# Kernel optimization log

Measured on AMD Instinct MI355X. Metric: run time of the kernel, lower is better.

The kernel has to match this reference:

```python
import jax, jax.numpy as jnp
import numpy as np

N = 50000      # nodes
E = 800000     # edges (avg degree 16)
D_IN = 128     # input_dim
H = 64         # hidden_dim (== output_dim)
L = 3          # num_layers


def setup_inputs() -> dict:
    key = jax.random.key(0)
    ks = jax.random.split(key, 24)
    s = 0.05
    p = lambda k, shape: jax.random.normal(k, shape, dtype=jnp.float32) * s
    inp = {}
    inp["node_features"] = jax.random.normal(ks[0], (N, D_IN), dtype=jnp.float32)
    inp["edge_index"] = jax.random.randint(ks[1], (2, E), 0, N, dtype=jnp.int32)
    # pre_mlp: Linear-ReLU-Linear (setup_LRL_nn with hidden_sizes=[hidden_dim])
    inp["pre_w1"] = p(ks[2], (D_IN, H)); inp["pre_b1"] = jnp.zeros((H,), jnp.float32)
    inp["pre_w2"] = p(ks[3], (H, H));    inp["pre_b2"] = jnp.zeros((H,), jnp.float32)
    # learnable skip gates (initialized to ones as in the module)
    inp["skip"] = jnp.ones((L, L), jnp.float32)
    # SAGEConv layers: lin_l (on mean-aggregated neighbors, with bias) + lin_r (root)
    for i in range(L):
        din = H * (i + 1)
        inp[f"wl{i}"] = p(ks[4 + 3 * i], (din, H))
        inp[f"bl{i}"] = jnp.zeros((H,), jnp.float32)
        inp[f"wr{i}"] = p(ks[5 + 3 * i], (din, H))
    # post_mlp: 256->64, 64->64, 64->256, 256->64
    inp["post_w1"] = p(ks[14], (H * (L + 1), H)); inp["post_b1"] = jnp.zeros((H,), jnp.float32)
    inp["post_w2"] = p(ks[15], (H, H));           inp["post_b2"] = jnp.zeros((H,), jnp.float32)
    inp["post_w3"] = p(ks[16], (H, 256));         inp["post_b3"] = jnp.zeros((256,), jnp.float32)
    inp["post_w4"] = p(ks[17], (256, H));         inp["post_b4"] = jnp.zeros((H,), jnp.float32)
    return inp


def _sage(x, src, dst, inv_deg, wl, bl, wr):
    # PyG SAGEConv (mean aggr): lin_l(mean_{j->i} x_j) + lin_r(x_i)
    agg = jax.ops.segment_sum(x[src], dst, num_segments=N) * inv_deg  # [N, Din]
    return agg @ wl + bl + x @ wr


def reference(node_features, edge_index,
              pre_w1, pre_b1, pre_w2, pre_b2, skip,
              wl0, bl0, wr0, wl1, bl1, wr1, wl2, bl2, wr2,
              post_w1, post_b1, post_w2, post_b2, post_w3, post_b3, post_w4, post_b4):
    src, dst = edge_index[0], edge_index[1]
    deg = jax.ops.segment_sum(jnp.ones((E,), jnp.float32), dst, num_segments=N)
    inv_deg = (1.0 / jnp.maximum(deg, 1.0))[:, None]  # [N,1]

    # pre_mlp
    x = jax.nn.relu(node_features @ pre_w1 + pre_b1) @ pre_w2 + pre_b2  # [N,H]

    layers = [(wl0, bl0, wr0), (wl1, bl1, wr1), (wl2, bl2, wr2)]
    all_emb = [x]
    emb = x
    for i, (wl, bl, wr) in enumerate(layers):
        gates = jax.nn.sigmoid(skip[i, :i + 1])  # [i+1]
        curr = jnp.concatenate([all_emb[j] * gates[j] for j in range(i + 1)], axis=1)  # [N, H*(i+1)]
        h = jax.nn.relu(_sage(curr, src, dst, inv_deg, wl, bl, wr))  # [N,H]  (dropout p=0)
        emb = jnp.concatenate([emb, h], axis=1)
        all_emb.append(h)

    s = jnp.sum(emb, axis=-2)  # sums over all nodes -> [H*(L+1)] (faithful to source)
    h = jax.nn.leaky_relu(s @ post_w1 + post_b1, negative_slope=0.1)
    h = jax.nn.relu(h @ post_w2 + post_b2)
    h = jax.nn.relu(h @ post_w3 + post_b3)
    return h @ post_w4 + post_b4  # [H]
```

## Files before the change

### kernel.cpp

```cpp
#include <hip/hip_runtime.h>
#include <math.h>

#define NN 50000
#define NE 800000
#define NB 196

typedef float v4f __attribute__((ext_vector_type(4)));
typedef float v2f __attribute__((ext_vector_type(2)));
typedef _Float16 v8h __attribute__((ext_vector_type(8)));

__device__ __forceinline__ unsigned char enc8(float v) {
#if __has_builtin(__builtin_amdgcn_cvt_pk_fp8_f32)
  return (unsigned char)(__builtin_amdgcn_cvt_pk_fp8_f32(v, v, 0, false) & 0xFF);
#else
  unsigned u = __float_as_uint(v);
  unsigned s = (u >> 24) & 0x80u;
  unsigned au = u & 0x7fffffffu;
  float a = __uint_as_float(au);
  if (au < 0x3C800000u) {
    int m = (int)(a * 512.0f + 0.5f);
    if (m >= 8) return (unsigned char)(s | 8u);
    return (unsigned char)(s | (unsigned)m);
  }
  unsigned r = au + 0x7FFFFu + ((au >> 20) & 1u);
  unsigned e = (r >> 23) - 120u;
  unsigned man = (r >> 20) & 7u;
  if (e > 15u) { e = 15u; man = 6u; }
  return (unsigned char)(s | (e << 3) | man);
#endif
}

#if __has_builtin(__builtin_amdgcn_cvt_pk_f32_fp8)
#define DEC8_HW 1
#else
__device__ __forceinline__ float dec8_1(unsigned b) {
  unsigned s = (b & 0x80u) << 24;
  unsigned em = b & 0x7fu;
  float v;
  if (em >= 8u) v = __uint_as_float((((em >> 3) + 120u) << 23) | ((em & 7u) << 20));
  else v = (float)em * 0.001953125f;
  return __uint_as_float(__float_as_uint(v) | s);
}
#endif

__device__ __forceinline__ void dec8x8(uint2 u, float* f) {
#ifdef DEC8_HW
  v2f p0 = __builtin_amdgcn_cvt_pk_f32_fp8((int)u.x, false);
  v2f p1 = __builtin_amdgcn_cvt_pk_f32_fp8((int)u.x, true);
  v2f p2 = __builtin_amdgcn_cvt_pk_f32_fp8((int)u.y, false);
  v2f p3 = __builtin_amdgcn_cvt_pk_f32_fp8((int)u.y, true);
  f[0] = p0.x; f[1] = p0.y; f[2] = p1.x; f[3] = p1.y;
  f[4] = p2.x; f[5] = p2.y; f[6] = p3.x; f[7] = p3.y;
#else
#pragma unroll
  for (int i = 0; i < 4; ++i) f[i] = dec8_1((u.x >> (8 * i)) & 0xFF);
#pragma unroll
  for (int i = 0; i < 4; ++i) f[4 + i] = dec8_1((u.y >> (8 * i)) & 0xFF);
#endif
}
__device__ __forceinline__ void dec8x16(uint4 u, float* f) {
  dec8x8(make_uint2(u.x, u.y), f);
  dec8x8(make_uint2(u.z, u.w), f + 8);
}


__global__ __launch_bounds__(256) void k_bhist(const int* __restrict__ dst,
                                               int* __restrict__ gbcnt) {
  __shared__ int lcnt[NB];
  int t = threadIdx.x;
  for (int i = t; i < NB; i += 256) lcnt[i] = 0;
  __syncthreads();
  int eb = blockIdx.x * 4096;
#pragma unroll
  for (int i = 0; i < 16; ++i) {
    int e = eb + i * 256 + t;
    if (e < NE) atomicAdd(&lcnt[dst[e] >> 8], 1);
  }
  __syncthreads();
  for (int i = t; i < NB; i += 256)
    if (lcnt[i]) atomicAdd(&gbcnt[i], lcnt[i]);
}

__global__ __launch_bounds__(256) void k_bscan(const int* __restrict__ gbcnt,
                                               int* __restrict__ boff,
                                               int* __restrict__ gcur,
                                               int* __restrict__ offs,
                                               float* __restrict__ sv) {
  __shared__ int sd[256];
  int t = threadIdx.x;
  sv[t] = 0.f;
  int v = (t < NB) ? gbcnt[t] : 0;
  sd[t] = v;
  __syncthreads();
  for (int o = 1; o < 256; o <<= 1) {
    int u = (t >= o) ? sd[t - o] : 0;
    __syncthreads();
    sd[t] += u;
    __syncthreads();
  }
  if (t < NB) { int x = sd[t] - v; boff[t] = x; gcur[t] = x; }
  if (t == NB - 1) boff[NB] = sd[t];
  if (t == 0) offs[NN] = NE;
}

__global__ __launch_bounds__(256) void k_bscatter(const int* __restrict__ src,
                                                  const int* __restrict__ dst,
                                                  int* __restrict__ gcur,
                                                  unsigned* __restrict__ ebuf) {
  __shared__ int cnt[NB];
  __shared__ int base[NB];
  int t = threadIdx.x;
  for (int i = t; i < NB; i += 256) cnt[i] = 0;
  __syncthreads();
  int eb = blockIdx.x * 4096;
  unsigned pk[16];
  int bk[16], lp[16];
#pragma unroll
  for (int i = 0; i < 16; ++i) {
    int e = eb + i * 256 + t;
    if (e < NE) {
      int d = dst[e];
      int b = d >> 8;
      pk[i] = ((unsigned)src[e] << 8) | (unsigned)(d & 255);
      bk[i] = b;
      lp[i] = atomicAdd(&cnt[b], 1);
    }
  }
  __syncthreads();
  for (int i = t; i < NB; i += 256)
    base[i] = cnt[i] ? atomicAdd(&gcur[i], cnt[i]) : 0;
  __syncthreads();
#pragma unroll
  for (int i = 0; i < 16; ++i) {
    int e = eb + i * 256 + t;
    if (e < NE) ebuf[base[bk[i]] + lp[i]] = pk[i];
  }
}

__global__ __launch_bounds__(256) void k_bbuild(const unsigned* __restrict__ ebuf,
                                                const int* __restrict__ boff,
                                                int* __restrict__ offs,
                                                float* __restrict__ invd,
                                                int* __restrict__ csr) {
  __shared__ int dcnt[256];
  __shared__ int cur[256];
  int t = threadIdx.x;
  int b = blockIdx.x;
  int node0 = b << 8;
  int es = boff[b], ee = boff[b + 1];
  dcnt[t] = 0;
  __syncthreads();
  for (int e = es + t; e < ee; e += 256) atomicAdd(&dcnt[ebuf[e] & 255], 1);
  __syncthreads();
  int v = dcnt[t];
  cur[t] = v;
  __syncthreads();
  for (int o = 1; o < 256; o <<= 1) {
    int u = (t >= o) ? cur[t - o] : 0;
    __syncthreads();
    cur[t] += u;
    __syncthreads();
  }
  int excl = cur[t] - v;
  int node = node0 + t;
  if (node < NN) {
    offs[node] = es + excl;
    invd[node] = 1.0f / fmaxf((float)v, 1.0f);
  }
  __syncthreads();
  cur[t] = es + excl;
  __syncthreads();
  for (int e = es + t; e < ee; e += 256) {
    unsigned pk = ebuf[e];
    int p = atomicAdd(&cur[pk & 255], 1);
    csr[p] = (int)(pk >> 8);
  }
}

struct LinArgs {
  const _Float16* a[6];
  const float* w[6];
  int gidx[6];
  int nsrc;
  int fusedsrc;
  const unsigned char* feat8;
  const int* offs;
  const int* csr;
  const float* invd;
  _Float16* mout;
  const float* bias;
  const float* skip;
  _Float16* outp;
  unsigned char* out8;
  float* colsum;
  int n;
  int relu;
};

__global__ __launch_bounds__(256) void k_linear(LinArgs A) {
  __shared__ _Float16 sW[2][2][64 * 72];
  __shared__ _Float16 atile[64 * 72];
  const int t    = threadIdx.x;
  const int lane = t & 63;
  const int wv   = t >> 6;
  const int qd   = lane >> 4;
  const int ln   = lane & 15;
  const int n0   = blockIdx.x * 64;

  const int sn = t & 63;
  float wreg[16];
  auto loadW = [&](int s) {
    const float* w = A.w[s];
#pragma unroll
    for (int c = 0; c < 2; ++c) {
      int kb = (wv + 4 * c) * 8;
#pragma unroll
      for (int j = 0; j < 8; ++j)
        wreg[c * 8 + j] = w[(size_t)(kb + j) * 64 + sn];
    }
  };
  auto writeW = [&](int s, int b) {
    float gs = 1.0f;
    if (A.gidx[s] >= 0) gs = 1.0f / (1.0f + __expf(-A.skip[A.gidx[s]]));
#pragma unroll
    for (int c = 0; c < 2; ++c) {
      int cb = wv + 4 * c;
      v8h hv, lv;
#pragma unroll
      for (int j = 0; j < 8; ++j) {
        float f = wreg[c * 8 + j] * gs;
        _Float16 h = (_Float16)f;
        hv[j] = h;
        lv[j] = (_Float16)(f - (float)h);
      }
      *(v8h*)(&sW[b][0][sn * 72 + cb * 8]) = hv;
      *(v8h*)(&sW[b][1][sn * 72 + cb * 8]) = lv;
    }
  };

  loadW(0);

  if (A.fusedsrc >= 0) {
    const int nd = t >> 2;
    const int q  = t & 3;
    const int node = n0 + nd;
    float a[16];
#pragma unroll
    for (int i = 0; i < 16; ++i) a[i] = 0.f;
    float dinv = 0.f;
    if (node < A.n) {
      int s = A.offs[node], e = A.offs[node + 1];
      dinv = A.invd[node];
      const unsigned char* fb = A.feat8;
      int p = s;
      for (; p + 4 <= e; p += 4) {
        int j0 = __builtin_nontemporal_load(A.csr + p);
        int j1 = __builtin_nontemporal_load(A.csr + p + 1);
        int j2 = __builtin_nontemporal_load(A.csr + p + 2);
        int j3 = __builtin_nontemporal_load(A.csr + p + 3);
        uint4 u0 = *(const uint4*)(fb + (size_t)j0 * 64 + q * 16);
        uint4 u1 = *(const uint4*)(fb + (size_t)j1 * 64 + q * 16);
        uint4 u2 = *(const uint4*)(fb + (size_t)j2 * 64 + q * 16);
        uint4 u3 = *(const uint4*)(fb + (size_t)j3 * 64 + q * 16);
        float f0[16], f1[16], f2[16], f3[16];
        dec8x16(u0, f0); dec8x16(u1, f1); dec8x16(u2, f2); dec8x16(u3, f3);
#pragma unroll
        for (int i = 0; i < 16; ++i) a[i] += (f0[i] + f1[i]) + (f2[i] + f3[i]);
      }
      for (; p < e; ++p) {
        int j = __builtin_nontemporal_load(A.csr + p);
        uint4 u = *(const uint4*)(fb + (size_t)j * 64 + q * 16);
        float f[16];
        dec8x16(u, f);
#pragma unroll
        for (int i = 0; i < 16; ++i) a[i] += f[i];
      }
    }
    v8h o0, o1;
#pragma unroll
    for (int i = 0; i < 8; ++i) {
      o0[i] = (_Float16)(a[i] * dinv);
      o1[i] = (_Float16)(a[8 + i] * dinv);
    }
    *(v8h*)(&atile[nd * 72 + q * 16]) = o0;
    *(v8h*)(&atile[nd * 72 + q * 16 + 8]) = o1;
    if (A.mout && node < A.n) {
      *(v8h*)(A.mout + (size_t)node * 64 + q * 16) = o0;
      *(v8h*)(A.mout + (size_t)node * 64 + q * 16 + 8) = o1;
    }
  }

  writeW(0, 0);
  __syncthreads();

  v4f acc[4];
#pragma unroll
  for (int ct = 0; ct < 4; ++ct) acc[ct] = (v4f){0.f, 0.f, 0.f, 0.f};

  const int arow = n0 + wv * 16 + ln;
  const bool arv = arow < A.n;
  v8h ah[2];
  auto loadA = [&](int s) {
    if (s == A.fusedsrc) {
      const _Float16* ph = atile + (wv * 16 + ln) * 72;
      ah[0] = *(const v8h*)(ph + qd * 8);
      ah[1] = *(const v8h*)(ph + 32 + qd * 8);
    } else if (arv) {
      const _Float16* ph = A.a[s] + (size_t)arow * 64;
#pragma unroll
      for (int ks = 0; ks < 2; ++ks)
        ah[ks] = *(const v8h*)(ph + ks * 32 + qd * 8);
    } else {
      v8h z;
#pragma unroll
      for (int j = 0; j < 8; ++j) z[j] = (_Float16)0.f;
      ah[0] = ah[1] = z;
    }
  };

  for (int s = 0; s < A.nsrc; ++s) {
    loadA(s);
    if (s + 1 < A.nsrc) loadW(s + 1);
    const _Float16* wh = &sW[s & 1][0][0];
    const _Float16* wl = &sW[s & 1][1][0];
#pragma unroll
    for (int ks = 0; ks < 2; ++ks) {
#pragma unroll
      for (int ct = 0; ct < 4; ++ct) {
        int wn = ct * 16 + ln;
        v8h bh = *(const v8h*)(wh + wn * 72 + ks * 32 + qd * 8);
        v8h bl = *(const v8h*)(wl + wn * 72 + ks * 32 + qd * 8);
        acc[ct] = __builtin_amdgcn_mfma_f32_16x16x32_f16(ah[ks], bh, acc[ct], 0, 0, 0);
        acc[ct] = __builtin_amdgcn_mfma_f32_16x16x32_f16(ah[ks], bl, acc[ct], 0, 0, 0);
      }
    }
    if (s + 1 < A.nsrc) writeW(s + 1, (s + 1) & 1);
    __syncthreads();
  }

  float bvals[4];
#pragma unroll
  for (int ct = 0; ct < 4; ++ct) bvals[ct] = A.bias[ct * 16 + ln];

  unsigned char* f8t = (unsigned char*)&sW[1][0][0];
  float* red = (float*)&sW[0][0][0];

  float cs[4] = {0.f, 0.f, 0.f, 0.f};
#pragma unroll
  for (int ct = 0; ct < 4; ++ct) {
#pragma unroll
    for (int r = 0; r < 4; ++r) {
      int nb = wv * 16 + qd * 4 + r;
      int node = n0 + nb;
      float v = acc[ct][r] + bvals[ct];
      if (A.relu) v = fmaxf(v, 0.f);
      if (node < A.n) {
        if (A.outp) A.outp[(size_t)node * 64 + ct * 16 + ln] = (_Float16)v;
        if (A.out8) f8t[nb * 64 + ct * 16 + ln] = enc8(v);
        cs[ct] += v;
      }
    }
  }
  if (A.colsum) {
#pragma unroll
    for (int ct = 0; ct < 4; ++ct) {
      float v = cs[ct];
      v += __shfl_xor(v, 16, 64);
      v += __shfl_xor(v, 32, 64);
      if (qd == 0) red[wv * 64 + ct * 16 + ln] = v;
    }
  }
  if (A.out8 || A.colsum) __syncthreads();
  if (A.out8) {
    int row = t >> 2, ch = t & 3;
    if (n0 + row < A.n) {
      uint4 val = *(const uint4*)(f8t + row * 64 + ch * 16);
      *(uint4*)(A.out8 + (size_t)(n0 + row) * 64 + ch * 16) = val;
    }
  }
  if (A.colsum && t < 64) {
    float ssum = red[t] + red[64 + t] + red[128 + t] + red[192 + t];
    atomicAdd(&A.colsum[t], ssum);
  }
}

__global__ __launch_bounds__(256) void k_pre(
    const float* __restrict__ nf,
    const float* __restrict__ w1, const float* __restrict__ b1,
    const float* __restrict__ w2, const float* __restrict__ b2,
    _Float16* __restrict__ xout, unsigned char* __restrict__ x8,
    float* __restrict__ colsum, int n) {
  __shared__ _Float16 sW[2][2][64 * 72];
  __shared__ _Float16 atile[64 * 72];
  const int t    = threadIdx.x;
  const int lane = t & 63;
  const int wv   = t >> 6;
  const int qd   = lane >> 4;
  const int ln   = lane & 15;
  const int n0   = blockIdx.x * 64;
  const int sn   = t & 63;

  float wreg[16];
  auto loadW = [&](const float* w) {
#pragma unroll
    for (int c = 0; c < 2; ++c) {
      int kb = (wv + 4 * c) * 8;
#pragma unroll
      for (int j = 0; j < 8; ++j)
        wreg[c * 8 + j] = w[(size_t)(kb + j) * 64 + sn];
    }
  };
  auto writeW = [&](int b) {
#pragma unroll
    for (int c = 0; c < 2; ++c) {
      int cb = wv + 4 * c;
      v8h hv, lv;
#pragma unroll
      for (int j = 0; j < 8; ++j) {
        float f = wreg[c * 8 + j];
        _Float16 h = (_Float16)f;
        hv[j] = h;
        lv[j] = (_Float16)(f - (float)h);
      }
      *(v8h*)(&sW[b][0][sn * 72 + cb * 8]) = hv;
      *(v8h*)(&sW[b][1][sn * 72 + cb * 8]) = lv;
    }
  };

  const int arow = n0 + wv * 16 + ln;
  const bool arv = arow < n;
  v4f acc[4];
#pragma unroll
  for (int ct = 0; ct < 4; ++ct) acc[ct] = (v4f){0.f, 0.f, 0.f, 0.f};
  v8h ah[2];

  auto loadAf32 = [&](const float* base) {
#pragma unroll
    for (int ks = 0; ks < 2; ++ks) {
      v8h hv;
      if (arv) {
        const float* p = base + (size_t)arow * 128 + ks * 32 + qd * 8;
        float4 u0 = *(const float4*)(p);
        float4 u1 = *(const float4*)(p + 4);
        hv[0] = (_Float16)u0.x; hv[1] = (_Float16)u0.y;
        hv[2] = (_Float16)u0.z; hv[3] = (_Float16)u0.w;
        hv[4] = (_Float16)u1.x; hv[5] = (_Float16)u1.y;
        hv[6] = (_Float16)u1.z; hv[7] = (_Float16)u1.w;
      } else {
#pragma unroll
        for (int j = 0; j < 8; ++j) hv[j] = (_Float16)0.f;
      }
      ah[ks] = hv;
    }
  };
  auto domfma = [&](int b) {
    const _Float16* wh = &sW[b][0][0];
    const _Float16* wl = &sW[b][1][0];
#pragma unroll
    for (int ks = 0; ks < 2; ++ks) {
#pragma unroll
      for (int ct = 0; ct < 4; ++ct) {
        int wn = ct * 16 + ln;
        v8h bh = *(const v8h*)(wh + wn * 72 + ks * 32 + qd * 8);
        v8h bl = *(const v8h*)(wl + wn * 72 + ks * 32 + qd * 8);
        acc[ct] = __builtin_amdgcn_mfma_f32_16x16x32_f16(ah[ks], bh, acc[ct], 0, 0, 0);
        acc[ct] = __builtin_amdgcn_mfma_f32_16x16x32_f16(ah[ks], bl, acc[ct], 0, 0, 0);
      }
    }
  };

  loadW(w1);
  writeW(0);
  __syncthreads();
  loadAf32(nf);
  loadW(w1 + 64 * 64);
  domfma(0);
  writeW(1);
  __syncthreads();
  loadAf32(nf + 64);
  loadW(w2);
  domfma(1);
  writeW(0);

  float b1v[4];
#pragma unroll
  for (int ct = 0; ct < 4; ++ct) b1v[ct] = b1[ct * 16 + ln];
#pragma unroll
  for (int ct = 0; ct < 4; ++ct) {
#pragma unroll
    for (int r = 0; r < 4; ++r) {
      int nb = wv * 16 + qd * 4 + r;
      float v = fmaxf(acc[ct][r] + b1v[ct], 0.f);
      atile[nb * 72 + ct * 16 + ln] = (_Float16)v;
    }
  }
#pragma unroll
  for (int ct = 0; ct < 4; ++ct) acc[ct] = (v4f){0.f, 0.f, 0.f, 0.f};
  __syncthreads();

  const int trow = wv * 16 + ln;
#pragma unroll
  for (int ks = 0; ks < 2; ++ks)
    ah[ks] = *(const v8h*)(atile + trow * 72 + ks * 32 + qd * 8);
  domfma(0);

  float b2v[4];
#pragma unroll
  for (int ct = 0; ct < 4; ++ct) b2v[ct] = b2[ct * 16 + ln];

  unsigned char* f8t = (unsigned char*)&sW[1][0][0];
  float* red = (float*)&sW[0][0][0];
  float cs[4] = {0.f, 0.f, 0.f, 0.f};
  __syncthreads();
#pragma unroll
  for (int ct = 0; ct < 4; ++ct) {
#pragma unroll
    for (int r = 0; r < 4; ++r) {
      int nb = wv * 16 + qd * 4 + r;
      int node = n0 + nb;
      float v = acc[ct][r] + b2v[ct];
      if (node < n) {
        xout[(size_t)node * 64 + ct * 16 + ln] = (_Float16)v;
        f8t[nb * 64 + ct * 16 + ln] = enc8(v);
        cs[ct] += v;
      }
    }
  }
#pragma unroll
  for (int ct = 0; ct < 4; ++ct) {
    float v = cs[ct];
    v += __shfl_xor(v, 16, 64);
    v += __shfl_xor(v, 32, 64);
    if (qd == 0) red[wv * 64 + ct * 16 + ln] = v;
  }
  __syncthreads();
  {
    int row = t >> 2, ch = t & 3;
    if (n0 + row < n) {
      uint4 val = *(const uint4*)(f8t + row * 64 + ch * 16);
      *(uint4*)(x8 + (size_t)(n0 + row) * 64 + ch * 16) = val;
    }
  }
  if (t < 64) {
    float ssum = red[t] + red[64 + t] + red[128 + t] + red[192 + t];
    atomicAdd(&colsum[t], ssum);
  }
}

__global__ __launch_bounds__(256) void k_post(const float* __restrict__ s,
                                              const float* __restrict__ w1, const float* __restrict__ b1,
                                              const float* __restrict__ w2, const float* __restrict__ b2,
                                              const float* __restrict__ w3, const float* __restrict__ b3,
                                              const float* __restrict__ w4, const float* __restrict__ b4,
                                              float* __restrict__ outp) {
  __shared__ float sh[256], h1[64], h2[64], h3[256];
  int t = threadIdx.x;
  sh[t] = s[t];
  __syncthreads();
  if (t < 64) {
    float a = b1[t];
    for (int k = 0; k < 256; ++k) a += sh[k] * w1[k * 64 + t];
    h1[t] = (a >= 0.f) ? a : 0.1f * a;
  }
  __syncthreads();
  if (t < 64) {
    float a = b2[t];
    for (int k = 0; k < 64; ++k) a += h1[k] * w2[k * 64 + t];
    h2[t] = fmaxf(a, 0.f);
  }
  __syncthreads();
  {
    float a = b3[t];
    for (int k = 0; k < 64; ++k) a += h2[k] * w3[k * 256 + t];
    h3[t] = fmaxf(a, 0.f);
  }
  __syncthreads();
  if (t < 64) {
    float a = b4[t];
    for (int k = 0; k < 256; ++k) a += h3[k] * w4[k * 64 + t];
    outp[t] = a;
  }
}

extern "C" void kernel_launch(void* const* d_in, const int* in_sizes, int n_in,
                              void* d_out, int out_size, void* d_ws, size_t ws_size,
                              hipStream_t stream) {
  const float* nf     = (const float*)d_in[0];
  const int*   ei     = (const int*)d_in[1];
  const float* pre_w1 = (const float*)d_in[2];
  const float* pre_b1 = (const float*)d_in[3];
  const float* pre_w2 = (const float*)d_in[4];
  const float* pre_b2 = (const float*)d_in[5];
  const float* skip   = (const float*)d_in[6];
  const float* wl0 = (const float*)d_in[7],  *bl0 = (const float*)d_in[8],  *wr0 = (const float*)d_in[9];
  const float* wl1 = (const float*)d_in[10], *bl1 = (const float*)d_in[11], *wr1 = (const float*)d_in[12];
  const float* wl2 = (const float*)d_in[13], *bl2 = (const float*)d_in[14], *wr2 = (const float*)d_in[15];
  const float* pw1 = (const float*)d_in[16], *pb1 = (const float*)d_in[17];
  const float* pw2 = (const float*)d_in[18], *pb2 = (const float*)d_in[19];
  const float* pw3 = (const float*)d_in[20], *pb3 = (const float*)d_in[21];
  const float* pw4 = (const float*)d_in[22], *pb4 = (const float*)d_in[23];
  float* out = (float*)d_out;

  const int N = NN, E = NE;

  char* ws = (char*)d_ws;
  size_t pos = 0;
  auto alloc = [&](size_t bytes) {
    char* p = ws + pos;
    pos += (bytes + 255) & ~(size_t)255;
    return (void*)p;
  };
  int*      gbcnt = (int*)alloc((size_t)NB * 4);
  int*      boff  = (int*)alloc((size_t)(NB + 1) * 4);
  int*      gcur  = (int*)alloc((size_t)NB * 4);
  unsigned* ebuf  = (unsigned*)alloc((size_t)E * 4);
  int*      offs  = (int*)alloc((size_t)(N + 1) * 4);
  float*    invd  = (float*)alloc((size_t)N * 4);
  int*      csr   = (int*)alloc((size_t)E * 4);
  const size_t PB = (size_t)N * 64 * 2;
  _Float16* x  = (_Float16*)alloc(PB);
  _Float16* h0 = (_Float16*)alloc(PB);
  _Float16* h1 = (_Float16*)alloc(PB);
  _Float16* m0 = (_Float16*)alloc(PB);
  _Float16* m1 = (_Float16*)alloc(PB);
  unsigned char* f8 = (unsigned char*)alloc((size_t)N * 64);
  float* sv = (float*)alloc(256 * 4);

  hipMemsetAsync(gbcnt, 0, (size_t)NB * 4, stream);

  const int* e_src = ei;
  const int* e_dst = ei + E;
  const int EGRID = (E + 4095) / 4096;
  k_bhist<<<EGRID, 256, 0, stream>>>(e_dst, gbcnt);
  k_bscan<<<1, 256, 0, stream>>>(gbcnt, boff, gcur, offs, sv);
  k_bscatter<<<EGRID, 256, 0, stream>>>(e_src, e_dst, gcur, ebuf);
  k_bbuild<<<NB, 256, 0, stream>>>(ebuf, boff, offs, invd, csr);

  const int LGRID = (N + 63) / 64;
  auto lin = [&](int nsrc, int fusedsrc, _Float16* mout,
                 const _Float16* a0, const float* w0, int g0,
                 const _Float16* a1, const float* w1_, int g1,
                 const _Float16* a2, const float* w2_, int g2,
                 const _Float16* a3, const float* w3_, int g3,
                 const _Float16* a4, const float* w4_, int g4,
                 const _Float16* a5, const float* w5_, int g5,
                 const float* bias, _Float16* op, unsigned char* o8,
                 float* colsum, int relu) {
    LinArgs A;
    A.a[0] = a0; A.a[1] = a1; A.a[2] = a2; A.a[3] = a3; A.a[4] = a4; A.a[5] = a5;
    A.w[0] = w0; A.w[1] = w1_; A.w[2] = w2_; A.w[3] = w3_; A.w[4] = w4_; A.w[5] = w5_;
    A.gidx[0] = g0; A.gidx[1] = g1; A.gidx[2] = g2; A.gidx[3] = g3; A.gidx[4] = g4; A.gidx[5] = g5;
    A.nsrc = nsrc; A.fusedsrc = fusedsrc;
    A.feat8 = f8; A.offs = offs; A.csr = csr; A.invd = invd;
    A.mout = mout;
    A.bias = bias; A.skip = skip;
    A.outp = op; A.out8 = o8; A.colsum = colsum;
    A.n = N; A.relu = relu;
    k_linear<<<LGRID, 256, 0, stream>>>(A);
  };

  k_pre<<<LGRID, 256, 0, stream>>>(nf, pre_w1, pre_b1, pre_w2, pre_b2,
                                   x, f8, sv, N);

  lin(2, 0, m0,
      nullptr, wl0, 0, x, wr0, 0,
      nullptr, nullptr, -1, nullptr, nullptr, -1,
      nullptr, nullptr, -1, nullptr, nullptr, -1,
      bl0, h0, f8, sv + 64, 1);

  lin(4, 1, m1,
      m0, wl1, 3, nullptr, wl1 + 64 * 64, 4,
      x, wr1, 3, h0, wr1 + 64 * 64, 4,
      nullptr, nullptr, -1, nullptr, nullptr, -1,
      bl1, h1, f8, sv + 128, 1);

  lin(6, 2, nullptr,
      m0, wl2, 6, m1, wl2 + 64 * 64, 7, nullptr, wl2 + 128 * 64, 8,
      x, wr2, 6, h0, wr2 + 64 * 64, 7, h1, wr2 + 128 * 64, 8,
      bl2, nullptr, nullptr, sv + 192, 1);

  k_post<<<1, 256, 0, stream>>>(sv, pw1, pb1, pw2, pb2, pw3, pb3, pw4, pb4, out);
}
```

Before: 333.2 us.

## Prepack gated split-fp16 weights once and double threads in linear kernel

```diff
diff --git a/kernel.cpp b/kernel.cpp
--- a/kernel.cpp
+++ b/kernel.cpp
@@ -4,6 +4,7 @@
 #define NN 50000
 #define NE 800000
 #define NB 196
+#define PBH 8192
 
 typedef float v4f __attribute__((ext_vector_type(4)));
 typedef float v2f __attribute__((ext_vector_type(2)));
@@ -177,10 +178,43 @@
   }
 }
 
+struct WPackArgs {
+  const float* w[15];
+  int gidx[15];
+  const float* skip;
+  _Float16* outp;
+};
+
+__global__ __launch_bounds__(256) void k_wpack(WPackArgs A) {
+  __shared__ float sw[4096];
+  int b = blockIdx.x, t = threadIdx.x;
+  const float* w = A.w[b];
+#pragma unroll
+  for (int i = 0; i < 4; ++i)
+    *(float4*)&sw[i * 1024 + t * 4] = *(const float4*)(w + i * 1024 + t * 4);
+  float gs = 1.f;
+  if (A.gidx[b] >= 0) gs = 1.f / (1.f + __expf(-A.skip[A.gidx[b]]));
+  __syncthreads();
+#pragma unroll
+  for (int i = 0; i < 4; ++i) {
+    int u = t * 4 + i;
+    int lane = u & 63, ct = (u >> 6) & 3, hl = (u >> 8) & 1, ks = (u >> 9) & 1;
+    v8h val;
+#pragma unroll
+    for (int j = 0; j < 8; ++j) {
+      int k = ks * 32 + ((lane >> 4) & 3) * 8 + j;
+      int n = ct * 16 + (lane & 15);
+      float f = sw[k * 64 + n] * gs;
+      _Float16 h = (_Float16)f;
+      val[j] = hl ? (_Float16)(f - (float)h) : h;
+    }
+    *(v8h*)(A.outp + (size_t)b * PBH + (size_t)u * 8) = val;
+  }
+}
+
 struct LinArgs {
   const _Float16* a[6];
-  const float* w[6];
-  int gidx[6];
+  int pb[6];
   int nsrc;
   int fusedsrc;
   const unsigned char* feat8;
@@ -188,8 +222,8 @@
   const int* csr;
   const float* invd;
   _Float16* mout;
+  const _Float16* wp;
   const float* bias;
-  const float* skip;
   _Float16* outp;
   unsigned char* out8;
   float* colsum;
@@ -197,8 +231,189 @@
   int relu;
 };
 
-__global__ __launch_bounds__(256) void k_linear(LinArgs A) {
-  __shared__ _Float16 sW[2][2][64 * 72];
+__global__ __launch_bounds__(512) void k_linear(LinArgs A) {
+  __shared__ _Float16 atile[64 * 72];
+  __shared__ float cbuf[64 * 65];
+  const int t    = threadIdx.x;
+  const int lane = t & 63;
+  const int w    = t >> 6;
+  const int wq   = w & 3;
+  const int sg   = w >> 2;
+  const int qd   = lane >> 4;
+  const int ln   = lane & 15;
+  const int n0   = blockIdx.x * 64;
+
+  if (A.fusedsrc >= 0) {
+    const int nd = t >> 3;
+    const int sl = (t >> 2) & 1;
+    const int q  = t & 3;
+    const int node = n0 + nd;
+    float a[16];
+#pragma unroll
+    for (int i = 0; i < 16; ++i) a[i] = 0.f;
+    float dinv = 0.f;
+    if (node < A.n) {
+      int s = A.offs[node], e = A.offs[node + 1];
+      dinv = A.invd[node];
+      const unsigned char* fb = A.feat8;
+      if (e > s) {
+        int emax = e - 1;
+        for (int p0 = s; p0 < e; p0 += 8) {
+          int pa = p0 + sl, pb_ = p0 + 2 + sl, pc = p0 + 4 + sl, pd = p0 + 6 + sl;
+          int ja = __builtin_nontemporal_load(A.csr + (pa < emax ? pa : emax));
+          int jb = __builtin_nontemporal_load(A.csr + (pb_ < emax ? pb_ : emax));
+          int jc = __builtin_nontemporal_load(A.csr + (pc < emax ? pc : emax));
+          int jd = __builtin_nontemporal_load(A.csr + (pd < emax ? pd : emax));
+          uint4 ua = *(const uint4*)(fb + (size_t)ja * 64 + q * 16);
+          uint4 ub = *(const uint4*)(fb + (size_t)jb * 64 + q * 16);
+          uint4 uc = *(const uint4*)(fb + (size_t)jc * 64 + q * 16);
+          uint4 ud = *(const uint4*)(fb + (size_t)jd * 64 + q * 16);
+          float f[16];
+          dec8x16(ua, f);
+          if (pa < e) {
+#pragma unroll
+            for (int i = 0; i < 16; ++i) a[i] += f[i];
+          }
+          dec8x16(ub, f);
+          if (pb_ < e) {
+#pragma unroll
+            for (int i = 0; i < 16; ++i) a[i] += f[i];
+          }
+          dec8x16(uc, f);
+          if (pc < e) {
+#pragma unroll
+            for (int i = 0; i < 16; ++i) a[i] += f[i];
+          }
+          dec8x16(ud, f);
+          if (pd < e) {
+#pragma unroll
+            for (int i = 0; i < 16; ++i) a[i] += f[i];
+          }
+        }
+      }
+    }
+#pragma unroll
+    for (int i = 0; i < 16; ++i) a[i] += __shfl_xor(a[i], 4, 64);
+    if (sl == 0) {
+      v8h o0, o1;
+#pragma unroll
+      for (int i = 0; i < 8; ++i) {
+        o0[i] = (_Float16)(a[i] * dinv);
+        o1[i] = (_Float16)(a[8 + i] * dinv);
+      }
+      *(v8h*)(&atile[nd * 72 + q * 16]) = o0;
+      *(v8h*)(&atile[nd * 72 + q * 16 + 8]) = o1;
+      if (A.mout && node < A.n) {
+        *(v8h*)(A.mout + (size_t)node * 64 + q * 16) = o0;
+        *(v8h*)(A.mout + (size_t)node * 64 + q * 16 + 8) = o1;
+      }
+    }
+  }
+  __syncthreads();
+
+  v4f acc[4];
+#pragma unroll
+  for (int ct = 0; ct < 4; ++ct) acc[ct] = (v4f){0.f, 0.f, 0.f, 0.f};
+
+  const int arow = n0 + wq * 16 + ln;
+  const bool arv = arow < A.n;
+  const int h = (A.nsrc + 1) >> 1;
+  const int sbeg = sg ? h : 0;
+  const int send = sg ? A.nsrc : h;
+  v8h ah[2];
+
+  for (int s = sbeg; s < send; ++s) {
+    if (s == A.fusedsrc) {
+      const _Float16* ph = atile + (wq * 16 + ln) * 72;
+      ah[0] = *(const v8h*)(ph + qd * 8);
+      ah[1] = *(const v8h*)(ph + 32 + qd * 8);
+    } else if (arv) {
+      const _Float16* ph = A.a[s] + (size_t)arow * 64;
+      ah[0] = *(const v8h*)(ph + qd * 8);
+      ah[1] = *(const v8h*)(ph + 32 + qd * 8);
+    } else {
+      v8h z;
+#pragma unroll
+      for (int j = 0; j < 8; ++j) z[j] = (_Float16)0.f;
+      ah[0] = ah[1] = z;
+    }
+    const _Float16* pw = A.wp + (size_t)A.pb[s] * PBH;
+#pragma unroll
+    for (int ks = 0; ks < 2; ++ks) {
+#pragma unroll
+      for (int ct = 0; ct < 4; ++ct) {
+        const _Float16* pf = pw + (size_t)(ks * 512 + ct * 64 + lane) * 8;
+        v8h bh = *(const v8h*)(pf);
+        v8h bl = *(const v8h*)(pf + 256 * 8);
+        acc[ct] = __builtin_amdgcn_mfma_f32_16x16x32_f16(ah[ks], bh, acc[ct], 0, 0, 0);
+        acc[ct] = __builtin_amdgcn_mfma_f32_16x16x32_f16(ah[ks], bl, acc[ct], 0, 0, 0);
+      }
+    }
+  }
+
+  if (sg == 1) {
+#pragma unroll
+    for (int ct = 0; ct < 4; ++ct)
+#pragma unroll
+      for (int r = 0; r < 4; ++r) {
+        int nb = wq * 16 + qd * 4 + r;
+        cbuf[nb * 65 + ct * 16 + ln] = acc[ct][r];
+      }
+  }
+  __syncthreads();
+
+  unsigned char* f8t = (unsigned char*)atile;
+  float* red = (float*)&atile[2304];
+
+  if (sg == 0) {
+    float bvals[4];
+#pragma unroll
+    for (int ct = 0; ct < 4; ++ct) bvals[ct] = A.bias[ct * 16 + ln];
+    float cs[4] = {0.f, 0.f, 0.f, 0.f};
+#pragma unroll
+    for (int ct = 0; ct < 4; ++ct) {
+#pragma unroll
+      for (int r = 0; r < 4; ++r) {
+        int nb = wq * 16 + qd * 4 + r;
+        int node = n0 + nb;
+        float v = acc[ct][r] + cbuf[nb * 65 + ct * 16 + ln] + bvals[ct];
+        if (A.relu) v = fmaxf(v, 0.f);
+        if (node < A.n) {
+          if (A.outp) A.outp[(size_t)node * 64 + ct * 16 + ln] = (_Float16)v;
+          if (A.out8) f8t[nb * 64 + ct * 16 + ln] = enc8(v);
+          cs[ct] += v;
+        }
+      }
+    }
+    if (A.colsum) {
+#pragma unroll
+      for (int ct = 0; ct < 4; ++ct) {
+        float v = cs[ct];
+        v += __shfl_xor(v, 16, 64);
+        v += __shfl_xor(v, 32, 64);
+        if (qd == 0) red[wq * 64 + ct * 16 + ln] = v;
+      }
+    }
+  }
+  if (A.out8 || A.colsum) __syncthreads();
+  if (A.out8 && t < 256) {
+    int row = t >> 2, ch = t & 3;
+    if (n0 + row < A.n) {
+      uint4 val = *(const uint4*)(f8t + row * 64 + ch * 16);
+      *(uint4*)(A.out8 + (size_t)(n0 + row) * 64 + ch * 16) = val;
+    }
+  }
+  if (A.colsum && t < 64) {
+    float ssum = red[t] + red[64 + t] + red[128 + t] + red[192 + t];
+    atomicAdd(&A.colsum[t], ssum);
+  }
+}
+
+__global__ __launch_bounds__(256) void k_pre(
+    const float* __restrict__ nf, const _Float16* __restrict__ wp,
+    const float* __restrict__ b1, const float* __restrict__ b2,
+    _Float16* __restrict__ xout, unsigned char* __restrict__ x8,
+    float* __restrict__ colsum, int n) {
   __shared__ _Float16 atile[64 * 72];
   const int t    = threadIdx.x;
   const int lane = t & 63;
@@ -206,240 +421,35 @@
   const int qd   = lane >> 4;
   const int ln   = lane & 15;
   const int n0   = blockIdx.x * 64;
-
-  const int sn = t & 63;
-  float wreg[16];
-  auto loadW = [&](int s) {
-    const float* w = A.w[s];
-#pragma unroll
-    for (int c = 0; c < 2; ++c) {
-      int kb = (wv + 4 * c) * 8;
-#pragma unroll
-      for (int j = 0; j < 8; ++j)
-        wreg[c * 8 + j] = w[(size_t)(kb + j) * 64 + sn];
-    }
-  };
-  auto writeW = [&](int s, int b) {
-    float gs = 1.0f;
-    if (A.gidx[s] >= 0) gs = 1.0f / (1.0f + __expf(-A.skip[A.gidx[s]]));
-#pragma unroll
-    for (int c = 0; c < 2; ++c) {
-      int cb = wv + 4 * c;
-      v8h hv, lv;
-#pragma unroll
-      for (int j = 0; j < 8; ++j) {
-        float f = wreg[c * 8 + j] * gs;
-        _Float16 h = (_Float16)f;
-        hv[j] = h;
-        lv[j] = (_Float16)(f - (float)h);
-      }
-      *(v8h*)(&sW[b][0][sn * 72 + cb * 8]) = hv;
-      *(v8h*)(&sW[b][1][sn * 72 + cb * 8]) = lv;
-    }
-  };
-
-  loadW(0);
-
-  if (A.fusedsrc >= 0) {
-    const int nd = t >> 2;
-    const int q  = t & 3;
-    const int node = n0 + nd;
-    float a[16];
-#pragma unroll
-    for (int i = 0; i < 16; ++i) a[i] = 0.f;
-    float dinv = 0.f;
-    if (node < A.n) {
-      int s = A.offs[node], e = A.offs[node + 1];
-      dinv = A.invd[node];
-      const unsigned char* fb = A.feat8;
-      int p = s;
-      for (; p + 4 <= e; p += 4) {
-        int j0 = __builtin_nontemporal_load(A.csr + p);
-        int j1 = __builtin_nontemporal_load(A.csr + p + 1);
-        int j2 = __builtin_nontemporal_load(A.csr + p + 2);
-        int j3 = __builtin_nontemporal_load(A.csr + p + 3);
-        uint4 u0 = *(const uint4*)(fb + (size_t)j0 * 64 + q * 16);
-        uint4 u1 = *(const uint4*)(fb + (size_t)j1 * 64 + q * 16);
-        uint4 u2 = *(const uint4*)(fb + (size_t)j2 * 64 + q * 16);
-        uint4 u3 = *(const uint4*)(fb + (size_t)j3 * 64 + q * 16);
-        float f0[16], f1[16], f2[16], f3[16];
-        dec8x16(u0, f0); dec8x16(u1, f1); dec8x16(u2, f2); dec8x16(u3, f3);
-#pragma unroll
-        for (int i = 0; i < 16; ++i) a[i] += (f0[i] + f1[i]) + (f2[i] + f3[i]);
-      }
-      for (; p < e; ++p) {
-        int j = __builtin_nontemporal_load(A.csr + p);
-        uint4 u = *(const uint4*)(fb + (size_t)j * 64 + q * 16);
-        float f[16];
-        dec8x16(u, f);
-#pragma unroll
-        for (int i = 0; i < 16; ++i) a[i] += f[i];
-      }
-    }
-    v8h o0, o1;
-#pragma unroll
-    for (int i = 0; i < 8; ++i) {
-      o0[i] = (_Float16)(a[i] * dinv);
-      o1[i] = (_Float16)(a[8 + i] * dinv);
-    }
-    *(v8h*)(&atile[nd * 72 + q * 16]) = o0;
-    *(v8h*)(&atile[nd * 72 + q * 16 + 8]) = o1;
-    if (A.mout && node < A.n) {
-      *(v8h*)(A.mout + (size_t)node * 64 + q * 16) = o0;
-      *(v8h*)(A.mout + (size_t)node * 64 + q * 16 + 8) = o1;
-    }
-  }
-
-  writeW(0, 0);
-  __syncthreads();
+  const int arow = n0 + wv * 16 + ln;
+  const bool arv = arow < n;
 
   v4f acc[4];
 #pragma unroll
   for (int ct = 0; ct < 4; ++ct) acc[ct] = (v4f){0.f, 0.f, 0.f, 0.f};
-
-  const int arow = n0 + wv * 16 + ln;
-  const bool arv = arow < A.n;
   v8h ah[2];
-  auto loadA = [&](int s) {
-    if (s == A.fusedsrc) {
-      const _Float16* ph = atile + (wv * 16 + ln) * 72;
-      ah[0] = *(const v8h*)(ph + qd * 8);
-      ah[1] = *(const v8h*)(ph + 32 + qd * 8);
-    } else if (arv) {
-      const _Float16* ph = A.a[s] + (size_t)arow * 64;
-#pragma unroll
-      for (int ks = 0; ks < 2; ++ks)
-        ah[ks] = *(const v8h*)(ph + ks * 32 + qd * 8);
-    } else {
-      v8h z;
-#pragma unroll
-      for (int j = 0; j < 8; ++j) z[j] = (_Float16)0.f;
-      ah[0] = ah[1] = z;
-    }
-  };
-
-  for (int s = 0; s < A.nsrc; ++s) {
-    loadA(s);
-    if (s + 1 < A.nsrc) loadW(s + 1);
-    const _Float16* wh = &sW[s & 1][0][0];
-    const _Float16* wl = &sW[s & 1][1][0];
+
+  auto domfma = [&](int pbi) {
+    const _Float16* pw = wp + (size_t)pbi * PBH;
 #pragma unroll
     for (int ks = 0; ks < 2; ++ks) {
 #pragma unroll
       for (int ct = 0; ct < 4; ++ct) {
-        int wn = ct * 16 + ln;
-        v8h bh = *(const v8h*)(wh + wn * 72 + ks * 32 + qd * 8);
-        v8h bl = *(const v8h*)(wl + wn * 72 + ks * 32 + qd * 8);
+        const _Float16* pf = pw + (size_t)(ks * 512 + ct * 64 + lane) * 8;
+        v8h bh = *(const v8h*)(pf);
+        v8h bl = *(const v8h*)(pf + 256 * 8);
         acc[ct] = __builtin_amdgcn_mfma_f32_16x16x32_f16(ah[ks], bh, acc[ct], 0, 0, 0);
         acc[ct] = __builtin_amdgcn_mfma_f32_16x16x32_f16(ah[ks], bl, acc[ct], 0, 0, 0);
       }
     }
-    if (s + 1 < A.nsrc) writeW(s + 1, (s + 1) & 1);
-    __syncthreads();
-  }
-
-  float bvals[4];
-#pragma unroll
-  for (int ct = 0; ct < 4; ++ct) bvals[ct] = A.bias[ct * 16 + ln];
-
-  unsigned char* f8t = (unsigned char*)&sW[1][0][0];
-  float* red = (float*)&sW[0][0][0];
-
-  float cs[4] = {0.f, 0.f, 0.f, 0.f};
-#pragma unroll
-  for (int ct = 0; ct < 4; ++ct) {
-#pragma unroll
-    for (int r = 0; r < 4; ++r) {
-      int nb = wv * 16 + qd * 4 + r;
-      int node = n0 + nb;
-      float v = acc[ct][r] + bvals[ct];
-      if (A.relu) v = fmaxf(v, 0.f);
-      if (node < A.n) {
-        if (A.outp) A.outp[(size_t)node * 64 + ct * 16 + ln] = (_Float16)v;
-        if (A.out8) f8t[nb * 64 + ct * 16 + ln] = enc8(v);
-        cs[ct] += v;
-      }
-    }
-  }
-  if (A.colsum) {
-#pragma unroll
-    for (int ct = 0; ct < 4; ++ct) {
-      float v = cs[ct];
-      v += __shfl_xor(v, 16, 64);
-      v += __shfl_xor(v, 32, 64);
-      if (qd == 0) red[wv * 64 + ct * 16 + ln] = v;
-    }
-  }
-  if (A.out8 || A.colsum) __syncthreads();
-  if (A.out8) {
-    int row = t >> 2, ch = t & 3;
-    if (n0 + row < A.n) {
-      uint4 val = *(const uint4*)(f8t + row * 64 + ch * 16);
-      *(uint4*)(A.out8 + (size_t)(n0 + row) * 64 + ch * 16) = val;
-    }
-  }
-  if (A.colsum && t < 64) {
-    float ssum = red[t] + red[64 + t] + red[128 + t] + red[192 + t];
-    atomicAdd(&A.colsum[t], ssum);
-  }
-}
-
-__global__ __launch_bounds__(256) void k_pre(
-    const float* __restrict__ nf,
-    const float* __restrict__ w1, const float* __restrict__ b1,
-    const float* __restrict__ w2, const float* __restrict__ b2,
-    _Float16* __restrict__ xout, unsigned char* __restrict__ x8,
-    float* __restrict__ colsum, int n) {
-  __shared__ _Float16 sW[2][2][64 * 72];
-  __shared__ _Float16 atile[64 * 72];
-  const int t    = threadIdx.x;
-  const int lane = t & 63;
-  const int wv   = t >> 6;
-  const int qd   = lane >> 4;
-  const int ln   = lane & 15;
-  const int n0   = blockIdx.x * 64;
-  const int sn   = t & 63;
-
-  float wreg[16];
-  auto loadW = [&](const float* w) {
-#pragma unroll
-    for (int c = 0; c < 2; ++c) {
-      int kb = (wv + 4 * c) * 8;
-#pragma unroll
-      for (int j = 0; j < 8; ++j)
-        wreg[c * 8 + j] = w[(size_t)(kb + j) * 64 + sn];
-    }
   };
-  auto writeW = [&](int b) {
-#pragma unroll
-    for (int c = 0; c < 2; ++c) {
-      int cb = wv + 4 * c;
-      v8h hv, lv;
-#pragma unroll
-      for (int j = 0; j < 8; ++j) {
-        float f = wreg[c * 8 + j];
-        _Float16 h = (_Float16)f;
-        hv[j] = h;
-        lv[j] = (_Float16)(f - (float)h);
-      }
-      *(v8h*)(&sW[b][0][sn * 72 + cb * 8]) = hv;
-      *(v8h*)(&sW[b][1][sn * 72 + cb * 8]) = lv;
-    }
-  };
-
-  const int arow = n0 + wv * 16 + ln;
-  const bool arv = arow < n;
-  v4f acc[4];
-#pragma unroll
-  for (int ct = 0; ct < 4; ++ct) acc[ct] = (v4f){0.f, 0.f, 0.f, 0.f};
-  v8h ah[2];
-
-  auto loadAf32 = [&](const float* base) {
+
+  for (int s = 0; s < 2; ++s) {
 #pragma unroll
     for (int ks = 0; ks < 2; ++ks) {
       v8h hv;
       if (arv) {
-        const float* p = base + (size_t)arow * 128 + ks * 32 + qd * 8;
+        const float* p = nf + (size_t)arow * 128 + s * 64 + ks * 32 + qd * 8;
         float4 u0 = *(const float4*)(p);
         float4 u1 = *(const float4*)(p + 4);
         hv[0] = (_Float16)u0.x; hv[1] = (_Float16)u0.y;
@@ -452,35 +462,8 @@
       }
       ah[ks] = hv;
     }
-  };
-  auto domfma = [&](int b) {
-    const _Float16* wh = &sW[b][0][0];
-    const _Float16* wl = &sW[b][1][0];
-#pragma unroll
-    for (int ks = 0; ks < 2; ++ks) {
-#pragma unroll
-      for (int ct = 0; ct < 4; ++ct) {
-        int wn = ct * 16 + ln;
-        v8h bh = *(const v8h*)(wh + wn * 72 + ks * 32 + qd * 8);
-        v8h bl = *(const v8h*)(wl + wn * 72 + ks * 32 + qd * 8);
-        acc[ct] = __builtin_amdgcn_mfma_f32_16x16x32_f16(ah[ks], bh, acc[ct], 0, 0, 0);
-        acc[ct] = __builtin_amdgcn_mfma_f32_16x16x32_f16(ah[ks], bl, acc[ct], 0, 0, 0);
-      }
-    }
-  };
-
-  loadW(w1);
-  writeW(0);
-  __syncthreads();
-  loadAf32(nf);
-  loadW(w1 + 64 * 64);
-  domfma(0);
-  writeW(1);
-  __syncthreads();
-  loadAf32(nf + 64);
-  loadW(w2);
-  domfma(1);
-  writeW(0);
+    domfma(s);
+  }
 
   float b1v[4];
 #pragma unroll
@@ -498,20 +481,21 @@
   for (int ct = 0; ct < 4; ++ct) acc[ct] = (v4f){0.f, 0.f, 0.f, 0.f};
   __syncthreads();
 
-  const int trow = wv * 16 + ln;
-#pragma unroll
-  for (int ks = 0; ks < 2; ++ks)
-    ah[ks] = *(const v8h*)(atile + trow * 72 + ks * 32 + qd * 8);
-  domfma(0);
+  {
+    const _Float16* ph = atile + (wv * 16 + ln) * 72;
+    ah[0] = *(const v8h*)(ph + qd * 8);
+    ah[1] = *(const v8h*)(ph + 32 + qd * 8);
+  }
+  domfma(2);
 
   float b2v[4];
 #pragma unroll
   for (int ct = 0; ct < 4; ++ct) b2v[ct] = b2[ct * 16 + ln];
 
-  unsigned char* f8t = (unsigned char*)&sW[1][0][0];
-  float* red = (float*)&sW[0][0][0];
+  __syncthreads();
+  unsigned char* f8t = (unsigned char*)atile;
+  float* red = (float*)&atile[2304];
   float cs[4] = {0.f, 0.f, 0.f, 0.f};
-  __syncthreads();
 #pragma unroll
   for (int ct = 0; ct < 4; ++ct) {
 #pragma unroll
@@ -624,9 +608,23 @@
   _Float16* m0 = (_Float16*)alloc(PB);
   _Float16* m1 = (_Float16*)alloc(PB);
   unsigned char* f8 = (unsigned char*)alloc((size_t)N * 64);
+  _Float16* wpk = (_Float16*)alloc((size_t)15 * PBH * 2);
   float* sv = (float*)alloc(256 * 4);
 
   hipMemsetAsync(gbcnt, 0, (size_t)NB * 4, stream);
+
+  {
+    WPackArgs W;
+    const float* wsrc[15] = {pre_w1, pre_w1 + 64 * 64, pre_w2,
+                             wl0, wr0,
+                             wl1, wl1 + 64 * 64, wr1, wr1 + 64 * 64,
+                             wl2, wl2 + 64 * 64, wl2 + 128 * 64,
+                             wr2, wr2 + 64 * 64, wr2 + 128 * 64};
+    const int gi[15] = {-1, -1, -1, 0, 0, 3, 4, 3, 4, 6, 7, 8, 6, 7, 8};
+    for (int i = 0; i < 15; ++i) { W.w[i] = wsrc[i]; W.gidx[i] = gi[i]; }
+    W.skip = skip; W.outp = wpk;
+    k_wpack<<<15, 256, 0, stream>>>(W);
+  }
 
   const int* e_src = ei;
   const int* e_dst = ei + E;
@@ -638,45 +636,36 @@
 
   const int LGRID = (N + 63) / 64;
   auto lin = [&](int nsrc, int fusedsrc, _Float16* mout,
-                 const _Float16* a0, const float* w0, int g0,
-                 const _Float16* a1, const float* w1_, int g1,
-                 const _Float16* a2, const float* w2_, int g2,
-                 const _Float16* a3, const float* w3_, int g3,
-                 const _Float16* a4, const float* w4_, int g4,
-                 const _Float16* a5, const float* w5_, int g5,
+                 const _Float16* a0, int p0, const _Float16* a1, int p1,
+                 const _Float16* a2, int p2, const _Float16* a3, int p3,
+                 const _Float16* a4, int p4, const _Float16* a5, int p5,
                  const float* bias, _Float16* op, unsigned char* o8,
                  float* colsum, int relu) {
     LinArgs A;
     A.a[0] = a0; A.a[1] = a1; A.a[2] = a2; A.a[3] = a3; A.a[4] = a4; A.a[5] = a5;
-    A.w[0] = w0; A.w[1] = w1_; A.w[2] = w2_; A.w[3] = w3_; A.w[4] = w4_; A.w[5] = w5_;
-    A.gidx[0] = g0; A.gidx[1] = g1; A.gidx[2] = g2; A.gidx[3] = g3; A.gidx[4] = g4; A.gidx[5] = g5;
+    A.pb[0] = p0; A.pb[1] = p1; A.pb[2] = p2; A.pb[3] = p3; A.pb[4] = p4; A.pb[5] = p5;
     A.nsrc = nsrc; A.fusedsrc = fusedsrc;
     A.feat8 = f8; A.offs = offs; A.csr = csr; A.invd = invd;
-    A.mout = mout;
-    A.bias = bias; A.skip = skip;
-    A.outp = op; A.out8 = o8; A.colsum = colsum;
+    A.mout = mout; A.wp = wpk;
+    A.bias = bias; A.outp = op; A.out8 = o8; A.colsum = colsum;
     A.n = N; A.relu = relu;
-    k_linear<<<LGRID, 256, 0, stream>>>(A);
+    k_linear<<<LGRID, 512, 0, stream>>>(A);
   };
 
-  k_pre<<<LGRID, 256, 0, stream>>>(nf, pre_w1, pre_b1, pre_w2, pre_b2,
-                                   x, f8, sv, N);
+  k_pre<<<LGRID, 256, 0, stream>>>(nf, wpk, pre_b1, pre_b2, x, f8, sv, N);
 
   lin(2, 0, m0,
-      nullptr, wl0, 0, x, wr0, 0,
-      nullptr, nullptr, -1, nullptr, nullptr, -1,
-      nullptr, nullptr, -1, nullptr, nullptr, -1,
+      nullptr, 3, x, 4,
+      nullptr, 0, nullptr, 0, nullptr, 0, nullptr, 0,
       bl0, h0, f8, sv + 64, 1);
 
   lin(4, 1, m1,
-      m0, wl1, 3, nullptr, wl1 + 64 * 64, 4,
-      x, wr1, 3, h0, wr1 + 64 * 64, 4,
-      nullptr, nullptr, -1, nullptr, nullptr, -1,
+      m0, 5, nullptr, 6, x, 7, h0, 8,
+      nullptr, 0, nullptr, 0,
       bl1, h1, f8, sv + 128, 1);
 
   lin(6, 2, nullptr,
-      m0, wl2, 6, m1, wl2 + 64 * 64, 7, nullptr, wl2 + 128 * 64, 8,
-      x, wr2, 6, h0, wr2 + 64 * 64, 7, h1, wr2 + 128 * 64, 8,
+      m0, 9, m1, 10, nullptr, 11, x, 12, h0, 13, h1, 14,
       bl2, nullptr, nullptr, sv + 192, 1);
 
   k_post<<<1, 256, 0, stream>>>(sv, pw1, pb1, pw2, pb2, pw3, pb3, pw4, pb4, out);
```

Measured after the change: 334.5 us. No clear change (+0.4%).
